# Optimization experiments

Measured on AMD Instinct MI355X. Metric: run time of the kernel, lower is better.

The kernel has to match this reference:

```python
import jax, jax.numpy as jnp
import numpy as np

N_NODES = 7
SIZE_X = 27
SIZE_X0 = 23
SIZE_H = 1024
SIZE_Z = 256
BATCH = 2048


def _gru(x, h, Wih, Whh, bih, bhh):
    # torch.nn.GRUCell math
    gi = x @ Wih.T + bih          # [B, 3H]
    gh = h @ Whh.T + bhh          # [B, 3H]
    ir, iz, inn = jnp.split(gi, 3, axis=-1)
    hr, hz, hn = jnp.split(gh, 3, axis=-1)
    r = jax.nn.sigmoid(ir + hr)
    z = jax.nn.sigmoid(iz + hz)
    n = jnp.tanh(inn + r * hn)
    return (1.0 - z) * n + z * h


def setup_inputs() -> dict:
    key = jax.random.key(0)
    ks = jax.random.split(key, 24)
    H, Xd, X0d, Zd = SIZE_H, SIZE_X, SIZE_X0, SIZE_Z

    def w(k, shape, fan):
        return jax.random.normal(k, shape, jnp.float32) / np.float32(np.sqrt(fan))

    inp = {}
    inp['X'] = jax.random.normal(ks[0], (BATCH, N_NODES, Xd), jnp.float32)
    inp['adj'] = jax.random.randint(ks[1], (BATCH, N_NODES, N_NODES), 0, 2, jnp.int32)
    # combin_encode GRUCell
    inp['W_ih_c'] = w(ks[2], (3 * H, Xd), H)
    inp['W_hh_c'] = w(ks[3], (3 * H, H), H)
    inp['b_ih_c'] = w(ks[4], (3 * H,), H)
    inp['b_hh_c'] = w(ks[5], (3 * H,), H)
    # loop_encode GRUCell
    inp['W_ih_l'] = w(ks[6], (3 * H, Xd), H)
    inp['W_hh_l'] = w(ks[7], (3 * H, H), H)
    inp['b_ih_l'] = w(ks[8], (3 * H,), H)
    inp['b_hh_l'] = w(ks[9], (3 * H,), H)
    # root_encode GRUCell (input size = size_X0)
    inp['W_ih_r'] = w(ks[10], (3 * H, X0d), H)
    inp['W_hh_r'] = w(ks[11], (3 * H, H), H)
    inp['b_ih_r'] = w(ks[12], (3 * H,), H)
    inp['b_hh_r'] = w(ks[13], (3 * H,), H)
    # gate: Linear(2H -> H) + sigmoid ; mapper: Linear(2H -> H, no bias)
    inp['Wg'] = w(ks[14], (H, 2 * H), 2 * H)
    inp['bg'] = w(ks[15], (H,), 2 * H)
    inp['Wm'] = w(ks[16], (H, 2 * H), 2 * H)
    # h_to_mu, h_to_std (Linear(H -> Z), std with softplus)
    inp['Wmu'] = w(ks[17], (Zd, H), H)
    inp['bmu'] = w(ks[18], (Zd,), H)
    inp['Wstd'] = w(ks[19], (Zd, H), H)
    inp['bstd'] = w(ks[20], (Zd,), H)
    return inp


def reference(X, adj,
              W_ih_c, W_hh_c, b_ih_c, b_hh_c,
              W_ih_l, W_hh_l, b_ih_l, b_hh_l,
              W_ih_r, W_hh_r, b_ih_r, b_hh_r,
              Wg, bg, Wm, Wmu, bmu, Wstd, bstd):
    B = X.shape[0]
    hidden = jnp.zeros((B, N_NODES, SIZE_H), X.dtype)
    # encode: nodes processed v = n-1 .. 0 (fixed small unrolled loop)
    for v in range(N_NODES - 1, -1, -1):
        if v == N_NODES - 1:
            H_in = jnp.zeros((B, SIZE_H), X.dtype)  # H_init = zeros
        else:
            H_nb = hidden[:, v + 1:, :]                    # [B, k, H] neighbors v+1..n-1
            pred = (adj[:, v + 1:, v] > 0)[..., None]       # edge x -> v
            succ = (adj[:, v, v + 1:] > 0)[..., None]       # edge v -> x
            Hcat = jnp.concatenate([jnp.where(pred, H_nb, 0.0),
                                    jnp.where(succ, H_nb, 0.0)], axis=-1)  # [B, k, 2H]
            g = jax.nn.sigmoid(jnp.einsum('bkf,hf->bkh', Hcat, Wg) + bg)
            m = jnp.einsum('bkf,hf->bkh', Hcat, Wm)
            H_in = (g * m).sum(axis=1)                      # gated sum over neighbors
        Xv = X[:, v]
        if v == 0:
            Hv = _gru(Xv[:, :SIZE_X0], H_in, W_ih_r, W_hh_r, b_ih_r, b_hh_r)
        else:
            Hv = _gru(Xv, H_in, W_ih_c, W_hh_c, b_ih_c, b_hh_c)
            self_loop = (adj[:, v, v] > 0)[:, None]
            X_loop = jnp.where(self_loop, Xv, 0.0)
            Hv = _gru(X_loop, Hv, W_ih_l, W_hh_l, b_ih_l, b_hh_l)
        hidden = hidden.at[:, v].set(Hv)
    Hg = hidden[:, 0]
    mu = Hg @ Wmu.T + bmu
    std = jax.nn.softplus(Hg @ Wstd.T + bstd)
    return mu, std
```

## Files before the change

kernel.cpp:

```cpp
#include <hip/hip_runtime.h>
#include <hip/hip_bf16.h>
#include <cmath>


typedef __hip_bfloat16 bf16;
typedef __attribute__((ext_vector_type(8))) short bf16x8;
typedef __attribute__((ext_vector_type(4))) float f32x4;

constexpr int BATCH = 2048;
constexpr int HD    = 1024;
constexpr int LDA   = 1056;
constexpr size_t BH = (size_t)BATCH * HD;

__device__ __forceinline__ bf16  f2bf(float v){ return __float2bfloat16(v); }
__device__ __forceinline__ float sigm(float x){ return 1.0f/(1.0f+__expf(-x)); }

__device__ __forceinline__ void async16(bf16* lds_wave_uniform, const bf16* g){
  __builtin_amdgcn_global_load_lds(
      (const __attribute__((address_space(1))) void*)g,
      (__attribute__((address_space(3))) void*)lds_wave_uniform, 16, 0, 0);
}
__device__ __forceinline__ void ld4f(const bf16* p, float* o){
  ushort4 u = *reinterpret_cast<const ushort4*>(p);
  o[0] = __uint_as_float(((unsigned)u.x)<<16);
  o[1] = __uint_as_float(((unsigned)u.y)<<16);
  o[2] = __uint_as_float(((unsigned)u.z)<<16);
  o[3] = __uint_as_float(((unsigned)u.w)<<16);
}
__device__ __forceinline__ void st4bf(bf16* p, const float* v){
  bf16 o[4] = {f2bf(v[0]), f2bf(v[1]), f2bf(v[2]), f2bf(v[3])};
  *reinterpret_cast<ushort4*>(p) = *reinterpret_cast<const ushort4*>(o);
}

__global__ __launch_bounds__(256) void pack_waug_i(
    const float* __restrict__ Whh, const float* __restrict__ Wih, int xw,
    bf16* __restrict__ out)
{
  int c = blockIdx.x;
  int h = c >> 2, g = c & 3;
  for (int ch = threadIdx.x; ch < 264; ch += 256){
    int f0 = ch*4;
    float v[4] = {0.f,0.f,0.f,0.f};
    if (f0 < 1024){
      if (g < 3){
        int src = (g==2) ? (2048+h) : (g*1024+h);
        const float4 t = *reinterpret_cast<const float4*>(Whh + (size_t)src*1024 + f0);
        v[0]=t.x; v[1]=t.y; v[2]=t.z; v[3]=t.w;
      }
    } else if (g != 2){
      int src = (g==0) ? h : (g==1) ? (1024+h) : (2048+h);
      int fx = f0 - 1024;
      #pragma unroll
      for (int j=0;j<4;++j) if (fx+j < xw) v[j] = Wih[(size_t)src*xw + fx + j];
    }
    st4bf(out + (size_t)c*LDA + f0, v);
  }
}

__global__ __launch_bounds__(256) void pack_wgm(const float* __restrict__ Wg,
    const float* __restrict__ Wm, bf16* __restrict__ outW){
  int i = blockIdx.x*256 + threadIdx.x;
  int c = i >> 8, f0 = (i & 255)*4;
  int j = c >> 10, h = c & 1023;
  const float* src = (j < 2) ? Wg : Wm;
  float4 t = *reinterpret_cast<const float4*>(src + (size_t)h*2048 + ((j & 1) ? 1024 : 0) + f0);
  float v[4] = {t.x,t.y,t.z,t.w};
  st4bf(outW + (size_t)c*1024 + f0, v);
}

__global__ __launch_bounds__(256) void pack_wms(const float* __restrict__ Wmu,
    const float* __restrict__ Wstd, bf16* __restrict__ outW){
  int i = blockIdx.x*256 + threadIdx.x;
  int c = i >> 8, f0 = (i & 255)*4;
  const float* src = (c < 256) ? (Wmu + (size_t)c*1024) : (Wstd + (size_t)(c-256)*1024);
  float4 t = *reinterpret_cast<const float4*>(src + f0);
  float v[4] = {t.x,t.y,t.z,t.w};
  st4bf(outW + (size_t)c*1024 + f0, v);
}

__global__ __launch_bounds__(256) void pack_xpad(const float* __restrict__ X,
    bf16* __restrict__ out){
  int i = blockIdx.x*256 + threadIdx.x;
  int f = i & 31, bv = i >> 5;
  int b = bv / 7, v = bv % 7;
  float val = (f < 27) ? X[((size_t)b*7 + v)*27 + f] : 0.f;
  out[((size_t)v*BATCH + b)*32 + f] = f2bf(val);
}
__global__ __launch_bounds__(256) void pack_xpr(const float* __restrict__ X,
    bf16* __restrict__ out){
  int i = blockIdx.x*256 + threadIdx.x;
  int f = i & 31, b = i >> 5;
  float val = (f < 23) ? X[(size_t)b*7*27 + f] : 0.f;
  out[(size_t)b*32 + f] = f2bf(val);
}

__global__ __launch_bounds__(256) void combine_k(
    const bf16* __restrict__ P, const int* __restrict__ adj,
    const float* __restrict__ bg, const bf16* __restrict__ tailsrc,
    bf16* __restrict__ Hin, int v)
{
  int t  = threadIdx.x;
  int b  = blockIdx.x*2 + (t>>7);
  int tl = t & 127;
  int h0 = tl*8;
  float acc[8] = {0,0,0,0,0,0,0,0};
  float bgv[8];
  { const float4 a = *reinterpret_cast<const float4*>(bg + h0);
    const float4 c = *reinterpret_cast<const float4*>(bg + h0 + 4);
    bgv[0]=a.x;bgv[1]=a.y;bgv[2]=a.z;bgv[3]=a.w;bgv[4]=c.x;bgv[5]=c.y;bgv[6]=c.z;bgv[7]=c.w; }
  for (int k=v+1;k<7;++k){
    bool p = adj[b*49 + k*7 + v] > 0;
    bool s = adj[b*49 + v*7 + k] > 0;
    if (!p && !s) continue;
    const bf16* base = P + (size_t)(k-1)*4*BH + (size_t)b*HD + h0;
    float g1[8], g2[8], m1[8], m2[8];
    ld4f(base,          g1); ld4f(base+4,        g1+4);
    ld4f(base+BH,       g2); ld4f(base+BH+4,     g2+4);
    ld4f(base+2*BH,     m1); ld4f(base+2*BH+4,   m1+4);
    ld4f(base+3*BH,     m2); ld4f(base+3*BH+4,   m2+4);
    #pragma unroll
    for (int u=0;u<8;++u){
      float gg = (p?g1[u]:0.f) + (s?g2[u]:0.f);
      float mm = (p?m1[u]:0.f) + (s?m2[u]:0.f);
      acc[u] += sigm(gg + bgv[u]) * mm;
    }
  }
  st4bf(Hin + (size_t)b*LDA + h0,     acc);
  st4bf(Hin + (size_t)b*LDA + h0 + 4, acc+4);
  if (tl < 4){
    const ushort4* s0 = reinterpret_cast<const ushort4*>(tailsrc + (size_t)b*32 + tl*8);
    ushort4* d0 = reinterpret_cast<ushort4*>(Hin + (size_t)b*LDA + 1024 + tl*8);
    d0[0] = s0[0]; d0[1] = s0[1];
  }
}

template<int MODE>
__global__ __launch_bounds__(256) void gemm_t(
    const bf16* __restrict__ A, const bf16* __restrict__ Bw,
    bf16* __restrict__ out, float* __restrict__ outF,
    const float* __restrict__ bias1, const float* __restrict__ bias2,
    const int* __restrict__ adj, const bf16* __restrict__ xpad,
    int lda, int ldb, int kb, int ktot, int v, int tailw, int swz)
{
  __shared__ __align__(16) bf16 S[64*136];
  bf16* As = S;
  bf16* Bs = S + 2048;
  const int tid  = threadIdx.x;
  int bx, by;
  if (swz){ int xcd = blockIdx.x & 7, s = blockIdx.x >> 3;
    bx = ((xcd & 1) << 4) | (s & 15);
    by = ((xcd >> 1) << 3) | (s >> 4);
  } else { bx = blockIdx.x; by = blockIdx.y; }
  const int rb0  = bx*64, n0 = by*128;
  const int lane = tid & 63, w = tid >> 6;
  const int quad = lane >> 4, l15 = lane & 15;
  const int sr   = lane >> 2, sc = (lane & 3)*8;

  const bf16* gA = A  + (size_t)(rb0 + w*16 + sr)*lda + sc;
  const bf16* gB = Bw + (size_t)(n0  + w*32 + sr)*ldb + sc;
  bf16* lA = As + w*512;
  bf16* lB = Bs + w*1024;

  f32x4 acc[4][2] = {};
  for (int k0 = kb; k0 < ktot; k0 += 32){
    async16(lA,       gA + k0);
    async16(lB,       gB + k0);
    async16(lB + 512, gB + k0 + (size_t)16*ldb);
    __syncthreads();
    bf16x8 af0 = *reinterpret_cast<const bf16x8*>(&As[(  0 + l15)*32 + quad*8]);
    bf16x8 af1 = *reinterpret_cast<const bf16x8*>(&As[( 16 + l15)*32 + quad*8]);
    bf16x8 af2 = *reinterpret_cast<const bf16x8*>(&As[( 32 + l15)*32 + quad*8]);
    bf16x8 af3 = *reinterpret_cast<const bf16x8*>(&As[( 48 + l15)*32 + quad*8]);
    bf16x8 bf0 = *reinterpret_cast<const bf16x8*>(&Bs[w*1024 + (     l15)*32 + quad*8]);
    bf16x8 bf1 = *reinterpret_cast<const bf16x8*>(&Bs[w*1024 + (16 + l15)*32 + quad*8]);
    acc[0][0] = __builtin_amdgcn_mfma_f32_16x16x32_bf16(af0, bf0, acc[0][0], 0,0,0);
    acc[0][1] = __builtin_amdgcn_mfma_f32_16x16x32_bf16(af0, bf1, acc[0][1], 0,0,0);
    acc[1][0] = __builtin_amdgcn_mfma_f32_16x16x32_bf16(af1, bf0, acc[1][0], 0,0,0);
    acc[1][1] = __builtin_amdgcn_mfma_f32_16x16x32_bf16(af1, bf1, acc[1][1], 0,0,0);
    acc[2][0] = __builtin_amdgcn_mfma_f32_16x16x32_bf16(af2, bf0, acc[2][0], 0,0,0);
    acc[2][1] = __builtin_amdgcn_mfma_f32_16x16x32_bf16(af2, bf1, acc[2][1], 0,0,0);
    acc[3][0] = __builtin_amdgcn_mfma_f32_16x16x32_bf16(af3, bf0, acc[3][0], 0,0,0);
    acc[3][1] = __builtin_amdgcn_mfma_f32_16x16x32_bf16(af3, bf1, acc[3][1], 0,0,0);
    __syncthreads();
  }

  if (MODE == 1 || MODE == 2){
    #pragma unroll
    for (int tm=0;tm<4;++tm)
      #pragma unroll
      for (int tn=0;tn<2;++tn)
        #pragma unroll
        for (int i=0;i<4;++i){
          int b = rb0 + tm*16 + quad*4 + i;
          int c = n0  + w*32 + tn*16 + l15;
          float val = acc[tm][tn][i];
          if (MODE == 1){
            out[((size_t)(c>>10)*BATCH + b)*HD + (c & 1023)] = f2bf(val);
          } else {
            if (c < 256){
              outF[(size_t)b*256 + c] = val + bias1[c];
            } else {
              val += bias2[c-256];
              val = fmaxf(val,0.f) + log1pf(__expf(-fabsf(val)));
              outF[(size_t)BATCH*256 + (size_t)b*256 + (c-256)] = val;
            }
          }
        }
    return;
  }

  #pragma unroll
  for (int tm=0;tm<4;++tm)
    #pragma unroll
    for (int tn=0;tn<2;++tn)
      #pragma unroll
      for (int i=0;i<4;++i){
        int r = tm*16 + quad*4 + i;
        int c = w*32 + tn*16 + l15;
        S[r*136 + c] = f2bf(acc[tm][tn][i]);
      }
  __syncthreads();
  {
    const int row = tid >> 2;
    const int hs  = (tid & 3)*8;
    const int b   = rb0 + row;
    const int hbase = by*32;
    bf16 hv[16];
    #pragma unroll
    for (int j4=0; j4<8; j4+=4){
      const int hg = hbase + hs + j4;
      float4 bir = *reinterpret_cast<const float4*>(bias1 + hg);
      float4 biz = *reinterpret_cast<const float4*>(bias1 + 1024 + hg);
      float4 bin = *reinterpret_cast<const float4*>(bias1 + 2048 + hg);
      float4 bhr = *reinterpret_cast<const float4*>(bias2 + hg);
      float4 bhz = *reinterpret_cast<const float4*>(bias2 + 1024 + hg);
      float4 bhn = *reinterpret_cast<const float4*>(bias2 + 2048 + hg);
      const float* p_ir = &bir.x; const float* p_iz = &biz.x; const float* p_in = &bin.x;
      const float* p_hr = &bhr.x; const float* p_hz = &bhz.x; const float* p_hn = &bhn.x;
      float ho[4];
      ld4f(A + (size_t)b*lda + hg, ho);
      #pragma unroll
      for (int jj=0; jj<4; ++jj){
        float g[4];
        ld4f(&S[row*136 + (hs + j4 + jj)*4], g);
        float r = sigm(g[0] + p_ir[jj] + p_hr[jj]);
        float z = sigm(g[1] + p_iz[jj] + p_hz[jj]);
        float n = tanhf(g[3] + p_in[jj] + r*(g[2] + p_hn[jj]));
        hv[j4+jj] = f2bf((1.f - z)*n + z*ho[jj]);
      }
    }
    *reinterpret_cast<uint4*>(out + (size_t)b*lda + hbase + hs) =
        *reinterpret_cast<const uint4*>(&hv[0]);
  }
  if (tailw && by == 0){
    const int b = rb0 + (tid>>2), f0 = (tid&3)*8;
    bool self = adj[b*49 + v*8] > 0;
    uint4 tv = {0u,0u,0u,0u};
    if (self) tv = *reinterpret_cast<const uint4*>(xpad + (size_t)b*32 + f0);
    *reinterpret_cast<uint4*>(out + (size_t)b*lda + 1024 + f0) = tv;
  }
}

extern "C" void kernel_launch(void* const* d_in, const int* in_sizes, int n_in,
                              void* d_out, int out_size, void* d_ws, size_t ws_size,
                              hipStream_t stream)
{
  const float* X    = (const float*)d_in[0];
  const int*   adj  = (const int*)  d_in[1];
  const float* Wihc = (const float*)d_in[2];
  const float* Whhc = (const float*)d_in[3];
  const float* bihc = (const float*)d_in[4];
  const float* bhhc = (const float*)d_in[5];
  const float* Wihl = (const float*)d_in[6];
  const float* Whhl = (const float*)d_in[7];
  const float* bihl = (const float*)d_in[8];
  const float* bhhl = (const float*)d_in[9];
  const float* Wihr = (const float*)d_in[10];
  const float* Whhr = (const float*)d_in[11];
  const float* bihr = (const float*)d_in[12];
  const float* bhhr = (const float*)d_in[13];
  const float* Wg   = (const float*)d_in[14];
  const float* bg   = (const float*)d_in[15];
  const float* Wm   = (const float*)d_in[16];
  const float* Wmu  = (const float*)d_in[17];
  const float* bmu  = (const float*)d_in[18];
  const float* Wstd = (const float*)d_in[19];
  const float* bstd = (const float*)d_in[20];
  float* out = (float*)d_out;

  bf16* P    = (bf16*)d_ws;
  bf16* Hin  = P    + 24*BH;
  bf16* Hva  = Hin  + (size_t)BATCH*LDA;
  bf16* Hvb  = Hva  + (size_t)BATCH*LDA;
  bf16* Wca  = Hvb  + (size_t)BATCH*LDA;
  bf16* Wla  = Wca  + (size_t)4096*LDA;
  bf16* Wra  = Wla  + (size_t)4096*LDA;
  bf16* Wgm  = Wra  + (size_t)4096*LDA;
  bf16* Wms  = Wgm  + (size_t)4096*1024;
  bf16* Xp   = Wms  + (size_t)512*1024;
  bf16* XpR  = Xp   + (size_t)7*BATCH*32;

  pack_waug_i<<<4096, 256, 0, stream>>>(Whhc, Wihc, 27, Wca);
  pack_waug_i<<<4096, 256, 0, stream>>>(Whhl, Wihl, 27, Wla);
  pack_waug_i<<<4096, 256, 0, stream>>>(Whhr, Wihr, 23, Wra);
  pack_wgm  <<<4096, 256, 0, stream>>>(Wg, Wm, Wgm);
  pack_wms  <<<512,  256, 0, stream>>>(Wmu, Wstd, Wms);
  pack_xpad <<<1792, 256, 0, stream>>>(X, Xp);
  pack_xpr  <<<256,  256, 0, stream>>>(X, XpR);

  for (int v=6; v>=1; --v){
    const bf16* xt = Xp + (size_t)v*BATCH*32;
    combine_k<<<1024, 256, 0, stream>>>(P, adj, bg, xt, Hin, v);
    gemm_t<0><<<1024, 256, 0, stream>>>(Hin, Wca, Hva, nullptr,
        bihc, bhhc, adj, xt, LDA, LDA, (v==6)?1024:0, 1056, v, 1, 1);
    gemm_t<0><<<1024, 256, 0, stream>>>(Hva, Wla, Hvb, nullptr,
        bihl, bhhl, adj, nullptr, LDA, LDA, 0, 1056, v, 0, 1);
    gemm_t<1><<<1024, 256, 0, stream>>>(Hvb, Wgm, P + (size_t)(v-1)*4*BH,
        nullptr, nullptr, nullptr, nullptr, nullptr, LDA, 1024, 0, 1024, 0, 0, 1);
  }
  combine_k<<<1024, 256, 0, stream>>>(P, adj, bg, XpR, Hin, 0);
  gemm_t<0><<<1024, 256, 0, stream>>>(Hin, Wra, Hva, nullptr,
      bihr, bhhr, adj, nullptr, LDA, LDA, 0, 1056, 0, 0, 1);
  gemm_t<2><<<dim3(32,4), 256, 0, stream>>>(Hva, Wms, nullptr, out,
      bmu, bstd, nullptr, nullptr, LDA, 1024, 0, 1024, 0, 0, 0);
}
```

Measured before the change: 823.1 us.

## Enlarge GEMM block tile to 128x128 with 2x2 wave layout

Grows the gemm_t block tile from 64x128 to 128x128, with each wave computing a 64x64 sub-tile (4x4 MFMAs) instead of 64x32, and halves the grid sizes to match. Each loaded A/B fragment is reused across more MFMAs, which cuts LDS and global traffic per FLOP. The epilogue, the XCD swizzle and the tail write are remapped to two threads per row. In exchange the block uses more accumulator registers and LDS, and there are half as many blocks (512 on 256 CUs), which may lower occupancy and leave load imbalance.

```diff
diff --git a/kernel.cpp b/kernel.cpp
--- a/kernel.cpp
+++ b/kernel.cpp
@@ -142,45 +142,45 @@
     const int* __restrict__ adj, const bf16* __restrict__ xpad,
     int lda, int ldb, int kb, int ktot, int v, int tailw, int swz)
 {
-  __shared__ __align__(16) bf16 S[64*136];
+  __shared__ __align__(16) bf16 S[128*138];
   bf16* As = S;
-  bf16* Bs = S + 2048;
+  bf16* Bs = S + 4096;
   const int tid  = threadIdx.x;
   int bx, by;
   if (swz){ int xcd = blockIdx.x & 7, s = blockIdx.x >> 3;
-    bx = ((xcd & 1) << 4) | (s & 15);
-    by = ((xcd >> 1) << 3) | (s >> 4);
+    bx = ((xcd & 1) << 3) | (s & 7);
+    by = ((xcd >> 1) << 3) | (s >> 3);
   } else { bx = blockIdx.x; by = blockIdx.y; }
-  const int rb0  = bx*64, n0 = by*128;
+  const int rb0  = bx*128, n0 = by*128;
   const int lane = tid & 63, w = tid >> 6;
   const int quad = lane >> 4, l15 = lane & 15;
   const int sr   = lane >> 2, sc = (lane & 3)*8;
-
-  const bf16* gA = A  + (size_t)(rb0 + w*16 + sr)*lda + sc;
+  const int wr   = w >> 1,    wc = w & 1;
+
+  const bf16* gA = A  + (size_t)(rb0 + w*32 + sr)*lda + sc;
   const bf16* gB = Bw + (size_t)(n0  + w*32 + sr)*ldb + sc;
-  bf16* lA = As + w*512;
+  bf16* lA = As + w*1024;
   bf16* lB = Bs + w*1024;
 
-  f32x4 acc[4][2] = {};
+  f32x4 acc[4][4] = {};
   for (int k0 = kb; k0 < ktot; k0 += 32){
     async16(lA,       gA + k0);
+    async16(lA + 512, gA + k0 + (size_t)16*lda);
     async16(lB,       gB + k0);
     async16(lB + 512, gB + k0 + (size_t)16*ldb);
     __syncthreads();
-    bf16x8 af0 = *reinterpret_cast<const bf16x8*>(&As[(  0 + l15)*32 + quad*8]);
-    bf16x8 af1 = *reinterpret_cast<const bf16x8*>(&As[( 16 + l15)*32 + quad*8]);
-    bf16x8 af2 = *reinterpret_cast<const bf16x8*>(&As[( 32 + l15)*32 + quad*8]);
-    bf16x8 af3 = *reinterpret_cast<const bf16x8*>(&As[( 48 + l15)*32 + quad*8]);
-    bf16x8 bf0 = *reinterpret_cast<const bf16x8*>(&Bs[w*1024 + (     l15)*32 + quad*8]);
-    bf16x8 bf1 = *reinterpret_cast<const bf16x8*>(&Bs[w*1024 + (16 + l15)*32 + quad*8]);
-    acc[0][0] = __builtin_amdgcn_mfma_f32_16x16x32_bf16(af0, bf0, acc[0][0], 0,0,0);
-    acc[0][1] = __builtin_amdgcn_mfma_f32_16x16x32_bf16(af0, bf1, acc[0][1], 0,0,0);
-    acc[1][0] = __builtin_amdgcn_mfma_f32_16x16x32_bf16(af1, bf0, acc[1][0], 0,0,0);
-    acc[1][1] = __builtin_amdgcn_mfma_f32_16x16x32_bf16(af1, bf1, acc[1][1], 0,0,0);
-    acc[2][0] = __builtin_amdgcn_mfma_f32_16x16x32_bf16(af2, bf0, acc[2][0], 0,0,0);
-    acc[2][1] = __builtin_amdgcn_mfma_f32_16x16x32_bf16(af2, bf1, acc[2][1], 0,0,0);
-    acc[3][0] = __builtin_amdgcn_mfma_f32_16x16x32_bf16(af3, bf0, acc[3][0], 0,0,0);
-    acc[3][1] = __builtin_amdgcn_mfma_f32_16x16x32_bf16(af3, bf1, acc[3][1], 0,0,0);
+    bf16x8 aa[4], bb[4];
+    #pragma unroll
+    for (int m=0;m<4;++m)
+      aa[m] = *reinterpret_cast<const bf16x8*>(&As[(wr*64 + m*16 + l15)*32 + quad*8]);
+    #pragma unroll
+    for (int n=0;n<4;++n)
+      bb[n] = *reinterpret_cast<const bf16x8*>(&Bs[(wc*64 + n*16 + l15)*32 + quad*8]);
+    #pragma unroll
+    for (int m=0;m<4;++m)
+      #pragma unroll
+      for (int n=0;n<4;++n)
+        acc[m][n] = __builtin_amdgcn_mfma_f32_16x16x32_bf16(aa[m], bb[n], acc[m][n], 0,0,0);
     __syncthreads();
   }
 
@@ -188,11 +188,11 @@
     #pragma unroll
     for (int tm=0;tm<4;++tm)
       #pragma unroll
-      for (int tn=0;tn<2;++tn)
+      for (int tn=0;tn<4;++tn)
         #pragma unroll
         for (int i=0;i<4;++i){
-          int b = rb0 + tm*16 + quad*4 + i;
-          int c = n0  + w*32 + tn*16 + l15;
+          int b = rb0 + wr*64 + tm*16 + quad*4 + i;
+          int c = n0  + wc*64 + tn*16 + l15;
           float val = acc[tm][tn][i];
           if (MODE == 1){
             out[((size_t)(c>>10)*BATCH + b)*HD + (c & 1023)] = f2bf(val);
@@ -212,23 +212,23 @@
   #pragma unroll
   for (int tm=0;tm<4;++tm)
     #pragma unroll
-    for (int tn=0;tn<2;++tn)
+    for (int tn=0;tn<4;++tn)
       #pragma unroll
       for (int i=0;i<4;++i){
-        int r = tm*16 + quad*4 + i;
-        int c = w*32 + tn*16 + l15;
-        S[r*136 + c] = f2bf(acc[tm][tn][i]);
+        int r = wr*64 + tm*16 + quad*4 + i;
+        int c = wc*64 + tn*16 + l15;
+        S[r*138 + c] = f2bf(acc[tm][tn][i]);
       }
   __syncthreads();
   {
-    const int row = tid >> 2;
-    const int hs  = (tid & 3)*8;
+    const int row = tid >> 1;
+    const int hof = (tid & 1)*16;
     const int b   = rb0 + row;
-    const int hbase = by*32;
+    const int hbase = by*32 + hof;
     bf16 hv[16];
     #pragma unroll
-    for (int j4=0; j4<8; j4+=4){
-      const int hg = hbase + hs + j4;
+    for (int j4=0; j4<16; j4+=4){
+      const int hg = hbase + j4;
       float4 bir = *reinterpret_cast<const float4*>(bias1 + hg);
       float4 biz = *reinterpret_cast<const float4*>(bias1 + 1024 + hg);
       float4 bin = *reinterpret_cast<const float4*>(bias1 + 2048 + hg);
@@ -242,22 +242,28 @@
       #pragma unroll
       for (int jj=0; jj<4; ++jj){
         float g[4];
-        ld4f(&S[row*136 + (hs + j4 + jj)*4], g);
+        ld4f(&S[row*138 + (hof + j4 + jj)*4], g);
         float r = sigm(g[0] + p_ir[jj] + p_hr[jj]);
         float z = sigm(g[1] + p_iz[jj] + p_hz[jj]);
         float n = tanhf(g[3] + p_in[jj] + r*(g[2] + p_hn[jj]));
         hv[j4+jj] = f2bf((1.f - z)*n + z*ho[jj]);
       }
     }
-    *reinterpret_cast<uint4*>(out + (size_t)b*lda + hbase + hs) =
+    *reinterpret_cast<uint4*>(out + (size_t)b*lda + hbase) =
         *reinterpret_cast<const uint4*>(&hv[0]);
+    *reinterpret_cast<uint4*>(out + (size_t)b*lda + hbase + 8) =
+        *reinterpret_cast<const uint4*>(&hv[8]);
   }
   if (tailw && by == 0){
-    const int b = rb0 + (tid>>2), f0 = (tid&3)*8;
-    bool self = adj[b*49 + v*8] > 0;
-    uint4 tv = {0u,0u,0u,0u};
-    if (self) tv = *reinterpret_cast<const uint4*>(xpad + (size_t)b*32 + f0);
-    *reinterpret_cast<uint4*>(out + (size_t)b*lda + 1024 + f0) = tv;
+    const int b2 = rb0 + (tid>>1), f0 = (tid&1)*16;
+    bool self = adj[b2*49 + v*8] > 0;
+    uint4 t0 = {0u,0u,0u,0u}, t1 = {0u,0u,0u,0u};
+    if (self){
+      const uint4* s0 = reinterpret_cast<const uint4*>(xpad + (size_t)b2*32 + f0);
+      t0 = s0[0]; t1 = s0[1];
+    }
+    uint4* d0 = reinterpret_cast<uint4*>(out + (size_t)b2*lda + 1024 + f0);
+    d0[0] = t0; d0[1] = t1;
   }
 }
 
@@ -311,16 +317,16 @@
   for (int v=6; v>=1; --v){
     const bf16* xt = Xp + (size_t)v*BATCH*32;
     combine_k<<<1024, 256, 0, stream>>>(P, adj, bg, xt, Hin, v);
-    gemm_t<0><<<1024, 256, 0, stream>>>(Hin, Wca, Hva, nullptr,
+    gemm_t<0><<<512, 256, 0, stream>>>(Hin, Wca, Hva, nullptr,
         bihc, bhhc, adj, xt, LDA, LDA, (v==6)?1024:0, 1056, v, 1, 1);
-    gemm_t<0><<<1024, 256, 0, stream>>>(Hva, Wla, Hvb, nullptr,
+    gemm_t<0><<<512, 256, 0, stream>>>(Hva, Wla, Hvb, nullptr,
         bihl, bhhl, adj, nullptr, LDA, LDA, 0, 1056, v, 0, 1);
-    gemm_t<1><<<1024, 256, 0, stream>>>(Hvb, Wgm, P + (size_t)(v-1)*4*BH,
+    gemm_t<1><<<512, 256, 0, stream>>>(Hvb, Wgm, P + (size_t)(v-1)*4*BH,
         nullptr, nullptr, nullptr, nullptr, nullptr, LDA, 1024, 0, 1024, 0, 0, 1);
   }
   combine_k<<<1024, 256, 0, stream>>>(P, adj, bg, XpR, Hin, 0);
-  gemm_t<0><<<1024, 256, 0, stream>>>(Hin, Wra, Hva, nullptr,
+  gemm_t<0><<<512, 256, 0, stream>>>(Hin, Wra, Hva, nullptr,
       bihr, bhhr, adj, nullptr, LDA, LDA, 0, 1056, 0, 0, 1);
-  gemm_t<2><<<dim3(32,4), 256, 0, stream>>>(Hva, Wms, nullptr, out,
+  gemm_t<2><<<dim3(16,4), 256, 0, stream>>>(Hva, Wms, nullptr, out,
       bmu, bstd, nullptr, nullptr, LDA, 1024, 0, 1024, 0, 0, 0);
 }
```

After: 909.6 us. 10.5% more time.

## Enlarge GEMM tile to 128x128 with 8 waves and double-buffered K=64 stages

Applied to the files above, without the earlier changes.

The GEMM kernel now uses 512-thread blocks with 8 waves arranged 2x4, computing 128x128 output tiles instead of 64x128. It double-buffers shared memory with a K step of 64 (two 32-wide sub-stages), so the async global-to-LDS copy of the next stage overlaps the MFMA work on the current one, and it cuts barriers to one per 64 of K. The grid is halved and the XCD swizzle adjusted. The cost is 64KB of LDS per block, which limits occupancy, and a larger epilogue footprint.

```diff
diff --git a/kernel.cpp b/kernel.cpp
--- a/kernel.cpp
+++ b/kernel.cpp
@@ -135,52 +135,89 @@
 }
 
 template<int MODE>
-__global__ __launch_bounds__(256) void gemm_t(
+__global__ __launch_bounds__(512, 4) void gemm_t(
     const bf16* __restrict__ A, const bf16* __restrict__ Bw,
     bf16* __restrict__ out, float* __restrict__ outF,
     const float* __restrict__ bias1, const float* __restrict__ bias2,
     const int* __restrict__ adj, const bf16* __restrict__ xpad,
     int lda, int ldb, int kb, int ktot, int v, int tailw, int swz)
 {
-  __shared__ __align__(16) bf16 S[64*136];
-  bf16* As = S;
-  bf16* Bs = S + 2048;
+  __shared__ __align__(16) bf16 S[32768];
   const int tid  = threadIdx.x;
   int bx, by;
   if (swz){ int xcd = blockIdx.x & 7, s = blockIdx.x >> 3;
-    bx = ((xcd & 1) << 4) | (s & 15);
-    by = ((xcd >> 1) << 3) | (s >> 4);
+    bx = ((xcd & 1) << 3) | (s & 7);
+    by = ((xcd >> 1) << 3) | (s >> 3);
   } else { bx = blockIdx.x; by = blockIdx.y; }
-  const int rb0  = bx*64, n0 = by*128;
+  const int rb0  = bx*128, n0 = by*128;
   const int lane = tid & 63, w = tid >> 6;
   const int quad = lane >> 4, l15 = lane & 15;
   const int sr   = lane >> 2, sc = (lane & 3)*8;
+  const int wr   = w >> 2,    wc = w & 3;
 
   const bf16* gA = A  + (size_t)(rb0 + w*16 + sr)*lda + sc;
-  const bf16* gB = Bw + (size_t)(n0  + w*32 + sr)*ldb + sc;
-  bf16* lA = As + w*512;
-  bf16* lB = Bs + w*1024;
+  const bf16* gB = Bw + (size_t)(n0  + w*16 + sr)*ldb + sc;
+  const int dA = w*512;
+  const int dB = 4096 + w*512;
+
+  const int nt = (ktot - kb + 63) >> 6;
+
+  {
+    async16(S + dA, gA + kb);
+    async16(S + dB, gB + kb);
+    if (ktot - kb > 32){
+      async16(S + 8192 + dA, gA + kb + 32);
+      async16(S + 8192 + dB, gB + kb + 32);
+    }
+  }
+  __syncthreads();
 
   f32x4 acc[4][2] = {};
-  for (int k0 = kb; k0 < ktot; k0 += 32){
-    async16(lA,       gA + k0);
-    async16(lB,       gB + k0);
-    async16(lB + 512, gB + k0 + (size_t)16*ldb);
-    __syncthreads();
-    bf16x8 af0 = *reinterpret_cast<const bf16x8*>(&As[(  0 + l15)*32 + quad*8]);
-    bf16x8 af1 = *reinterpret_cast<const bf16x8*>(&As[( 16 + l15)*32 + quad*8]);
-    bf16x8 af2 = *reinterpret_cast<const bf16x8*>(&As[( 32 + l15)*32 + quad*8]);
-    bf16x8 af3 = *reinterpret_cast<const bf16x8*>(&As[( 48 + l15)*32 + quad*8]);
-    bf16x8 bf0 = *reinterpret_cast<const bf16x8*>(&Bs[w*1024 + (     l15)*32 + quad*8]);
-    bf16x8 bf1 = *reinterpret_cast<const bf16x8*>(&Bs[w*1024 + (16 + l15)*32 + quad*8]);
-    acc[0][0] = __builtin_amdgcn_mfma_f32_16x16x32_bf16(af0, bf0, acc[0][0], 0,0,0);
-    acc[0][1] = __builtin_amdgcn_mfma_f32_16x16x32_bf16(af0, bf1, acc[0][1], 0,0,0);
-    acc[1][0] = __builtin_amdgcn_mfma_f32_16x16x32_bf16(af1, bf0, acc[1][0], 0,0,0);
-    acc[1][1] = __builtin_amdgcn_mfma_f32_16x16x32_bf16(af1, bf1, acc[1][1], 0,0,0);
-    acc[2][0] = __builtin_amdgcn_mfma_f32_16x16x32_bf16(af2, bf0, acc[2][0], 0,0,0);
-    acc[2][1] = __builtin_amdgcn_mfma_f32_16x16x32_bf16(af2, bf1, acc[2][1], 0,0,0);
-    acc[3][0] = __builtin_amdgcn_mfma_f32_16x16x32_bf16(af3, bf0, acc[3][0], 0,0,0);
-    acc[3][1] = __builtin_amdgcn_mfma_f32_16x16x32_bf16(af3, bf1, acc[3][1], 0,0,0);
+  for (int t = 0; t < nt; ++t){
+    const int k0 = kb + t*64;
+    if (t + 1 < nt){
+      bf16* bp = S + ((t+1)&1)*16384;
+      const int k1 = k0 + 64;
+      async16(bp + dA, gA + k1);
+      async16(bp + dB, gB + k1);
+      if (ktot - k1 > 32){
+        async16(bp + 8192 + dA, gA + k1 + 32);
+        async16(bp + 8192 + dB, gB + k1 + 32);
+      }
+    }
+    const bf16* buf = S + (t&1)*16384;
+    {
+      const bf16* As = buf;
+      const bf16* Bs = buf + 4096;
+      bf16x8 aa[4], bb[2];
+      #pragma unroll
+      for (int m=0;m<4;++m)
+        aa[m] = *reinterpret_cast<const bf16x8*>(&As[(wr*64 + m*16 + l15)*32 + quad*8]);
+      #pragma unroll
+      for (int n=0;n<2;++n)
+        bb[n] = *reinterpret_cast<const bf16x8*>(&Bs[(wc*32 + n*16 + l15)*32 + quad*8]);
+      #pragma unroll
+      for (int m=0;m<4;++m)
+        #pragma unroll
+        for (int n=0;n<2;++n)
+          acc[m][n] = __builtin_amdgcn_mfma_f32_16x16x32_bf16(aa[m], bb[n], acc[m][n], 0,0,0);
+    }
+    if (ktot - k0 > 32){
+      const bf16* As = buf + 8192;
+      const bf16* Bs = buf + 12288;
+      bf16x8 aa[4], bb[2];
+      #pragma unroll
+      for (int m=0;m<4;++m)
+        aa[m] = *reinterpret_cast<const bf16x8*>(&As[(wr*64 + m*16 + l15)*32 + quad*8]);
+      #pragma unroll
+      for (int n=0;n<2;++n)
+        bb[n] = *reinterpret_cast<const bf16x8*>(&Bs[(wc*32 + n*16 + l15)*32 + quad*8]);
+      #pragma unroll
+      for (int m=0;m<4;++m)
+        #pragma unroll
+        for (int n=0;n<2;++n)
+          acc[m][n] = __builtin_amdgcn_mfma_f32_16x16x32_bf16(aa[m], bb[n], acc[m][n], 0,0,0);
+    }
     __syncthreads();
   }
 
@@ -191,8 +228,8 @@
       for (int tn=0;tn<2;++tn)
         #pragma unroll
         for (int i=0;i<4;++i){
-          int b = rb0 + tm*16 + quad*4 + i;
-          int c = n0  + w*32 + tn*16 + l15;
+          int b = rb0 + wr*64 + tm*16 + quad*4 + i;
+          int c = n0  + wc*32 + tn*16 + l15;
           float val = acc[tm][tn][i];
           if (MODE == 1){
             out[((size_t)(c>>10)*BATCH + b)*HD + (c & 1023)] = f2bf(val);
@@ -215,8 +252,8 @@
     for (int tn=0;tn<2;++tn)
       #pragma unroll
       for (int i=0;i<4;++i){
-        int r = tm*16 + quad*4 + i;
-        int c = w*32 + tn*16 + l15;
+        int r = wr*64 + tm*16 + quad*4 + i;
+        int c = wc*32 + tn*16 + l15;
         S[r*136 + c] = f2bf(acc[tm][tn][i]);
       }
   __syncthreads();
@@ -253,11 +290,11 @@
         *reinterpret_cast<const uint4*>(&hv[0]);
   }
   if (tailw && by == 0){
-    const int b = rb0 + (tid>>2), f0 = (tid&3)*8;
-    bool self = adj[b*49 + v*8] > 0;
+    const int b2 = rb0 + (tid>>2), f0 = (tid&3)*8;
+    bool self = adj[b2*49 + v*8] > 0;
     uint4 tv = {0u,0u,0u,0u};
-    if (self) tv = *reinterpret_cast<const uint4*>(xpad + (size_t)b*32 + f0);
-    *reinterpret_cast<uint4*>(out + (size_t)b*lda + 1024 + f0) = tv;
+    if (self) tv = *reinterpret_cast<const uint4*>(xpad + (size_t)b2*32 + f0);
+    *reinterpret_cast<uint4*>(out + (size_t)b2*lda + 1024 + f0) = tv;
   }
 }
 
@@ -311,16 +348,16 @@
   for (int v=6; v>=1; --v){
     const bf16* xt = Xp + (size_t)v*BATCH*32;
     combine_k<<<1024, 256, 0, stream>>>(P, adj, bg, xt, Hin, v);
-    gemm_t<0><<<1024, 256, 0, stream>>>(Hin, Wca, Hva, nullptr,
+    gemm_t<0><<<512, 512, 0, stream>>>(Hin, Wca, Hva, nullptr,
         bihc, bhhc, adj, xt, LDA, LDA, (v==6)?1024:0, 1056, v, 1, 1);
-    gemm_t<0><<<1024, 256, 0, stream>>>(Hva, Wla, Hvb, nullptr,
+    gemm_t<0><<<512, 512, 0, stream>>>(Hva, Wla, Hvb, nullptr,
         bihl, bhhl, adj, nullptr, LDA, LDA, 0, 1056, v, 0, 1);
-    gemm_t<1><<<1024, 256, 0, stream>>>(Hvb, Wgm, P + (size_t)(v-1)*4*BH,
+    gemm_t<1><<<512, 512, 0, stream>>>(Hvb, Wgm, P + (size_t)(v-1)*4*BH,
         nullptr, nullptr, nullptr, nullptr, nullptr, LDA, 1024, 0, 1024, 0, 0, 1);
   }
   combine_k<<<1024, 256, 0, stream>>>(P, adj, bg, XpR, Hin, 0);
-  gemm_t<0><<<1024, 256, 0, stream>>>(Hin, Wra, Hva, nullptr,
+  gemm_t<0><<<512, 512, 0, stream>>>(Hin, Wra, Hva, nullptr,
       bihr, bhhr, adj, nullptr, LDA, LDA, 0, 1056, 0, 0, 1);
-  gemm_t<2><<<dim3(32,4), 256, 0, stream>>>(Hva, Wms, nullptr, out,
+  gemm_t<2><<<dim3(16,4), 512, 0, stream>>>(Hva, Wms, nullptr, out,
       bmu, bstd, nullptr, nullptr, LDA, 1024, 0, 1024, 0, 0, 0);
 }
```

Result: faster. 676.0 us (median of 2 runs) (-17.9%).
